# Kernel optimization log

Measured on AMD Instinct MI355X. Metric: run time of the kernel, lower is better.

The kernel has to match this reference:

```python
import jax, jax.numpy as jnp
import numpy as np


def setup_inputs() -> dict:
    key = jax.random.key(0)
    x = jax.random.normal(key, (8, 512, 96, 96), dtype=jnp.float32)
    gamma = jnp.zeros((1,), dtype=jnp.float32)  # Scale(0) learnable scalar
    return {"x": x, "gamma": gamma}


def reference(x, gamma):
    b, c, h, w = x.shape
    y = x.reshape(b, c, h * w)                      # [B, C, N]
    # channel-channel Gram matrix: [B, C, C]
    att = jnp.einsum('bcn,bdn->bcd', y, y)
    # DANet variant: softmax of (rowmax - scores)
    att = jnp.max(att, axis=-1, keepdims=True) - att
    att = jax.nn.softmax(att, axis=-1)
    # attention-weighted aggregation over channels: [B, C, N]
    feat = jnp.einsum('bcd,bdn->bcn', att, y).reshape(b, c, h, w)
    return gamma * feat + x
```

## Files before the change

kernel.cpp:

```cpp
#include <hip/hip_runtime.h>


typedef __attribute__((ext_vector_type(8))) short short8;
typedef __attribute__((ext_vector_type(4))) float f32x4;

#define GT 128
#define BK 64
#define LDA 72
#define NSPLIT 8
#define FBSPLIT 4

__device__ inline unsigned short f2bf(float f) {
    unsigned u = __builtin_bit_cast(unsigned, f);
    u += 0x7fffu + ((u >> 16) & 1u);
    return (unsigned short)(u >> 16);
}
__device__ inline unsigned permpack(float a, float b) {
    return __builtin_amdgcn_perm(__builtin_bit_cast(unsigned, b),
                                 __builtin_bit_cast(unsigned, a), 0x07060302u);
}
__device__ inline void gload_lds16(const short* g, short* l) {
    __builtin_amdgcn_global_load_lds(
        (const __attribute__((address_space(1))) void*)(g),
        (__attribute__((address_space(3))) void*)(l), 16, 0, 0);
}

__global__ __launch_bounds__(256) void tobf16_kernel(const float* __restrict__ x,
                                                     short* __restrict__ ybf) {
    const size_t total = (size_t)8 * 512 * 9216 / 8;
    const size_t stride = (size_t)gridDim.x * 256;
    for (size_t i = (size_t)blockIdx.x * 256 + threadIdx.x; i < total; i += stride) {
        const float4 a = ((const float4*)x)[2 * i];
        const float4 b = ((const float4*)x)[2 * i + 1];
        uint4 pv;
        pv.x = permpack(a.x, a.y);
        pv.y = permpack(a.z, a.w);
        pv.z = permpack(b.x, b.y);
        pv.w = permpack(b.z, b.w);
        ((uint4*)ybf)[i] = pv;
    }
}

__global__ __launch_bounds__(256, 2) void gram_kernel4(const short* __restrict__ ybf,
                                                       float* __restrict__ part) {
    const int C = 512, N = 9216;
    __shared__ short As[2][GT * BK];
    __shared__ short Bs[2][GT * BK];
    const int id = blockIdx.x;
    const int batch = id & 7;
    const int slot = id >> 3;
    const int split = slot / 10;
    const int pair = slot % 10;
    const int i_ = (pair < 4) ? 0 : (pair < 7) ? 1 : (pair < 9) ? 2 : 3;
    const int j_ = pair - ((i_ == 0) ? 0 : (i_ == 1) ? 3 : (i_ == 2) ? 5 : 6);
    const bool diag = (i_ == j_);
    const int c0 = i_ * GT, d0 = j_ * GT;
    const short* Y = ybf + (size_t)batch * C * N;
    const int t = threadIdx.x;
    const int w = t >> 6, l = t & 63;
    const int mw = (w >> 1) * 64, nw = (w & 1) * 64;
    const int lr = l & 15, lq = l >> 4;

    const int kw = N / NSPLIT;
    const int kbeg = split * kw;
    const int nt = kw / BK;

    auto STAGE = [&](int ti, int buf) {
        const int k0 = kbeg + ti * BK;
        #pragma unroll
        for (int p = 0; p < 4; ++p) {
            const int u = t + p * 256;
            const int row = u >> 3;
            const int us = (u ^ row) & 7;
            gload_lds16(Y + (size_t)(c0 + row) * N + k0 + us * 8, &As[buf][u * 8]);
        }
        if (!diag) {
            #pragma unroll
            for (int p = 0; p < 4; ++p) {
                const int u = t + p * 256;
                const int row = u >> 3;
                const int us = (u ^ row) & 7;
                gload_lds16(Y + (size_t)(d0 + row) * N + k0 + us * 8, &Bs[buf][u * 8]);
            }
        }
    };

    f32x4 acc[4][4] = {};
    STAGE(0, 0);
    __syncthreads();
    int cur = 0;
    for (int ti = 0; ti < nt; ++ti) {
        if (ti + 1 < nt) STAGE(ti + 1, cur ^ 1);
        const short* Acur = &As[cur][0];
        const short* Bcur = diag ? &As[cur][0] : &Bs[cur][0];
        #pragma unroll
        for (int h = 0; h < 2; ++h) {
            short8 af[4], bf[4];
            #pragma unroll
            for (int i = 0; i < 4; i++) {
                const int r = mw + i * 16 + lr;
                af[i] = *(const short8*)&Acur[r * BK + (((h * 4 + lq) ^ (r & 7)) * 8)];
            }
            #pragma unroll
            for (int j = 0; j < 4; j++) {
                const int r = nw + j * 16 + lr;
                bf[j] = *(const short8*)&Bcur[r * BK + (((h * 4 + lq) ^ (r & 7)) * 8)];
            }
            #pragma unroll
            for (int i = 0; i < 4; i++)
                #pragma unroll
                for (int j = 0; j < 4; j++)
                    acc[i][j] = __builtin_amdgcn_mfma_f32_16x16x32_bf16(af[i], bf[j], acc[i][j], 0, 0, 0);
        }
        __syncthreads();
        cur ^= 1;
    }
    float* P = part + ((size_t)batch * NSPLIT + split) * C * C;
    #pragma unroll
    for (int i = 0; i < 4; i++)
        #pragma unroll
        for (int j = 0; j < 4; j++)
            #pragma unroll
            for (int r = 0; r < 4; r++) {
                const int row = c0 + mw + i * 16 + lq * 4 + r;
                const int col = d0 + nw + j * 16 + lr;
                const float v = acc[i][j][r];
                P[(size_t)row * C + col] = v;
                if (!diag) P[(size_t)col * C + row] = v;
            }
}

__global__ __launch_bounds__(256) void rsoftmax_kernel(const float* __restrict__ part,
                                                       unsigned short* __restrict__ attbf) {
    const int C = 512;
    const int b = blockIdx.x >> 9;
    const int row = blockIdx.x & 511;
    const float* P0 = part + (size_t)b * NSPLIT * C * C + (size_t)row * C;
    const int t = threadIdx.x;
    float v0 = 0.f, v1 = 0.f;
    #pragma unroll
    for (int s = 0; s < NSPLIT; ++s) {
        const float* Ps = P0 + (size_t)s * C * C;
        v0 += Ps[t];
        v1 += Ps[t + 256];
    }

    float mn = fminf(v0, v1);
    #pragma unroll
    for (int off = 32; off > 0; off >>= 1) mn = fminf(mn, __shfl_xor(mn, off));
    __shared__ float redmin[4];
    const int wid = t >> 6, lane = t & 63;
    if (lane == 0) redmin[wid] = mn;
    __syncthreads();
    mn = fminf(fminf(redmin[0], redmin[1]), fminf(redmin[2], redmin[3]));

    const float e0 = expf(mn - v0), e1 = expf(mn - v1);
    float s = e0 + e1;
    #pragma unroll
    for (int off = 32; off > 0; off >>= 1) s += __shfl_xor(s, off);
    __shared__ float redsum[4];
    if (lane == 0) redsum[wid] = s;
    __syncthreads();
    s = redsum[0] + redsum[1] + redsum[2] + redsum[3];

    const float inv = 1.0f / s;
    unsigned short* A16 = attbf + (size_t)b * C * C + (size_t)row * C;
    A16[t] = f2bf(e0 * inv);
    A16[t + 256] = f2bf(e1 * inv);
}

__global__ __launch_bounds__(256, 2) void feat_kernel4(const short* __restrict__ attbf,
                                                       const short* __restrict__ ybf,
                                                       const float* __restrict__ x,
                                                       const float* __restrict__ gamma,
                                                       float* __restrict__ out) {
    const int C = 512, N = 9216;
    __shared__ short As[2][GT * BK];
    __shared__ short Bs[2][GT * BK];
    const int id = blockIdx.x;
    const int b = id & 7;
    const int slot = id >> 3;
    const int n0 = (slot >> 2) * GT;
    const int c0 = (slot & 3) * GT;
    const short* Ab = attbf + (size_t)b * C * C;
    const short* Y = ybf + (size_t)b * C * N;
    const int t = threadIdx.x;
    const int w = t >> 6, l = t & 63;
    const int mw = (w >> 1) * 64, nw = (w & 1) * 64;
    const int lr = l & 15, lq = l >> 4;
    const int ng = t & 31, kg = t >> 5;

    const int nt = C / BK;

    auto ASTAGE = [&](int ti, int buf) {
        const int k0 = ti * BK;
        #pragma unroll
        for (int p = 0; p < 4; ++p) {
            const int u = t + p * 256;
            const int row = u >> 3;
            const int us = (u ^ row) & 7;
            gload_lds16(Ab + (size_t)(c0 + row) * C + k0 + us * 8, &As[buf][u * 8]);
        }
    };

    uint2 rr[8];
    auto BLOAD = [&](int ti) {
        const short* pB = Y + (size_t)(ti * BK + kg * 8) * N + n0 + ng * 4;
        #pragma unroll
        for (int r = 0; r < 8; ++r) rr[r] = *(const uint2*)(pB + (size_t)r * N);
    };
    auto BWRITE = [&](int buf) {
        #pragma unroll
        for (int j = 0; j < 4; ++j) {
            const unsigned sel = (j & 1) ? 0x07060302u : 0x05040100u;
            unsigned w0, w1, w2, w3;
            if (j < 2) {
                w0 = __builtin_amdgcn_perm(rr[1].x, rr[0].x, sel);
                w1 = __builtin_amdgcn_perm(rr[3].x, rr[2].x, sel);
                w2 = __builtin_amdgcn_perm(rr[5].x, rr[4].x, sel);
                w3 = __builtin_amdgcn_perm(rr[7].x, rr[6].x, sel);
            } else {
                w0 = __builtin_amdgcn_perm(rr[1].y, rr[0].y, sel);
                w1 = __builtin_amdgcn_perm(rr[3].y, rr[2].y, sel);
                w2 = __builtin_amdgcn_perm(rr[5].y, rr[4].y, sel);
                w3 = __builtin_amdgcn_perm(rr[7].y, rr[6].y, sel);
            }
            const int nrow = ng * 4 + j;
            uint4 cv; cv.x = w0; cv.y = w1; cv.z = w2; cv.w = w3;
            *(uint4*)&Bs[buf][nrow * BK + ((kg ^ (nrow & 7)) * 8)] = cv;
        }
    };

    f32x4 acc[4][4] = {};
    BLOAD(0);
    ASTAGE(0, 0);
    BWRITE(0);
    __syncthreads();
    int cur = 0;
    for (int ti = 0; ti < nt; ++ti) {
        if (ti + 1 < nt) {
            BLOAD(ti + 1);
            ASTAGE(ti + 1, cur ^ 1);
        }
        #pragma unroll
        for (int h = 0; h < 2; ++h) {
            short8 af[4], bf[4];
            #pragma unroll
            for (int i = 0; i < 4; i++) {
                const int r = mw + i * 16 + lr;
                af[i] = *(const short8*)&As[cur][r * BK + (((h * 4 + lq) ^ (r & 7)) * 8)];
            }
            #pragma unroll
            for (int j = 0; j < 4; j++) {
                const int r = nw + j * 16 + lr;
                bf[j] = *(const short8*)&Bs[cur][r * BK + (((h * 4 + lq) ^ (r & 7)) * 8)];
            }
            #pragma unroll
            for (int i = 0; i < 4; i++)
                #pragma unroll
                for (int j = 0; j < 4; j++)
                    acc[i][j] = __builtin_amdgcn_mfma_f32_16x16x32_bf16(af[i], bf[j], acc[i][j], 0, 0, 0);
        }
        if (ti + 1 < nt) BWRITE(cur ^ 1);
        __syncthreads();
        cur ^= 1;
    }

    const float g = gamma[0];
    float* O = out + (size_t)b * C * N;
    const float* X = x + (size_t)b * C * N;
    #pragma unroll
    for (int i = 0; i < 4; i++)
        #pragma unroll
        for (int j = 0; j < 4; j++)
            #pragma unroll
            for (int r = 0; r < 4; r++) {
                const int row = c0 + mw + i * 16 + lq * 4 + r;
                const int col = n0 + nw + j * 16 + lr;
                const size_t idx = (size_t)row * N + col;
                O[idx] = g * acc[i][j][r] + X[idx];
            }
}

__global__ __launch_bounds__(256, 2) void gram_kernel3(const short* __restrict__ ybf,
                                                       float* __restrict__ att) {
    const int C = 512, N = 9216;
    __shared__ short As[2][GT * BK];
    __shared__ short Bs[2][GT * BK];
    const int id = blockIdx.x;
    const int batch = id & 7;
    const int slot = id >> 3;
    const int split = slot / 10;
    const int pair = slot % 10;
    const int i_ = (pair < 4) ? 0 : (pair < 7) ? 1 : (pair < 9) ? 2 : 3;
    const int j_ = pair - ((i_ == 0) ? 0 : (i_ == 1) ? 3 : (i_ == 2) ? 5 : 6);
    const bool diag = (i_ == j_);
    const int c0 = i_ * GT, d0 = j_ * GT;
    const short* Y = ybf + (size_t)batch * C * N;
    const int t = threadIdx.x;
    const int w = t >> 6, l = t & 63;
    const int mw = (w >> 1) * 64, nw = (w & 1) * 64;
    const int lr = l & 15, lq = l >> 4;

    const int kw = N / NSPLIT;
    const int kbeg = split * kw;
    const int nt = kw / BK;

    auto STAGE = [&](int ti, int buf) {
        const int k0 = kbeg + ti * BK;
        #pragma unroll
        for (int p = 0; p < 4; ++p) {
            const int u = t + p * 256;
            const int row = u >> 3;
            const int us = (u ^ row) & 7;
            gload_lds16(Y + (size_t)(c0 + row) * N + k0 + us * 8, &As[buf][u * 8]);
        }
        if (!diag) {
            #pragma unroll
            for (int p = 0; p < 4; ++p) {
                const int u = t + p * 256;
                const int row = u >> 3;
                const int us = (u ^ row) & 7;
                gload_lds16(Y + (size_t)(d0 + row) * N + k0 + us * 8, &Bs[buf][u * 8]);
            }
        }
    };

    f32x4 acc[4][4] = {};
    STAGE(0, 0);
    __syncthreads();
    int cur = 0;
    for (int ti = 0; ti < nt; ++ti) {
        if (ti + 1 < nt) STAGE(ti + 1, cur ^ 1);
        const short* Acur = &As[cur][0];
        const short* Bcur = diag ? &As[cur][0] : &Bs[cur][0];
        #pragma unroll
        for (int h = 0; h < 2; ++h) {
            short8 af[4], bf[4];
            #pragma unroll
            for (int i = 0; i < 4; i++) {
                const int r = mw + i * 16 + lr;
                af[i] = *(const short8*)&Acur[r * BK + (((h * 4 + lq) ^ (r & 7)) * 8)];
            }
            #pragma unroll
            for (int j = 0; j < 4; j++) {
                const int r = nw + j * 16 + lr;
                bf[j] = *(const short8*)&Bcur[r * BK + (((h * 4 + lq) ^ (r & 7)) * 8)];
            }
            #pragma unroll
            for (int i = 0; i < 4; i++)
                #pragma unroll
                for (int j = 0; j < 4; j++)
                    acc[i][j] = __builtin_amdgcn_mfma_f32_16x16x32_bf16(af[i], bf[j], acc[i][j], 0, 0, 0);
        }
        __syncthreads();
        cur ^= 1;
    }
    float* S = att + (size_t)batch * C * C;
    #pragma unroll
    for (int i = 0; i < 4; i++)
        #pragma unroll
        for (int j = 0; j < 4; j++)
            #pragma unroll
            for (int r = 0; r < 4; r++) {
                const int row = c0 + mw + i * 16 + lq * 4 + r;
                const int col = d0 + nw + j * 16 + lr;
                const float v = acc[i][j][r];
                unsafeAtomicAdd(&S[(size_t)row * C + col], v);
                if (!diag) unsafeAtomicAdd(&S[(size_t)col * C + row], v);
            }
}

__global__ __launch_bounds__(256) void softmax_kernel(float* __restrict__ att) {
    const int C = 512;
    float* S = att + (size_t)blockIdx.x * C;
    const int t = threadIdx.x;
    const float v0 = S[t], v1 = S[t + 256];

    float mn = fminf(v0, v1);
    #pragma unroll
    for (int off = 32; off > 0; off >>= 1) mn = fminf(mn, __shfl_xor(mn, off));
    __shared__ float redmin[4];
    const int wid = t >> 6, lane = t & 63;
    if (lane == 0) redmin[wid] = mn;
    __syncthreads();
    mn = fminf(fminf(redmin[0], redmin[1]), fminf(redmin[2], redmin[3]));

    const float e0 = expf(mn - v0), e1 = expf(mn - v1);
    float s = e0 + e1;
    #pragma unroll
    for (int off = 32; off > 0; off >>= 1) s += __shfl_xor(s, off);
    __shared__ float redsum[4];
    if (lane == 0) redsum[wid] = s;
    __syncthreads();
    s = redsum[0] + redsum[1] + redsum[2] + redsum[3];

    const float inv = 1.0f / s;
    unsigned short* S16 = (unsigned short*)S;
    S16[t] = f2bf(e0 * inv);
    S16[t + 256] = f2bf(e1 * inv);
}

__global__ __launch_bounds__(256, 2) void feat_kernel3(const float* __restrict__ att,
                                                       const short* __restrict__ ybf,
                                                       const float* __restrict__ x,
                                                       const float* __restrict__ gamma,
                                                       float* __restrict__ out) {
    const int C = 512, N = 9216;
    __shared__ short As[2][GT * BK];
    __shared__ short Bs[2][GT * BK];
    const int id = blockIdx.x;
    const int b = id & 7;
    const int slot = id >> 3;
    const int n0 = (slot >> 2) * GT;
    const int c0 = (slot & 3) * GT;
    const short* Ab = (const short*)(att + (size_t)b * C * C);
    const short* Y = ybf + (size_t)b * C * N;
    const int t = threadIdx.x;
    const int w = t >> 6, l = t & 63;
    const int mw = (w >> 1) * 64, nw = (w & 1) * 64;
    const int lr = l & 15, lq = l >> 4;
    const int ng = t & 31, kg = t >> 5;

    const int nt = C / BK;

    auto ASTAGE = [&](int ti, int buf) {
        const int k0 = ti * BK;
        #pragma unroll
        for (int p = 0; p < 4; ++p) {
            const int u = t + p * 256;
            const int row = u >> 3;
            const int us = (u ^ row) & 7;
            gload_lds16(Ab + (size_t)(c0 + row) * 1024 + k0 + us * 8, &As[buf][u * 8]);
        }
    };

    uint2 rr[8];
    auto BLOAD = [&](int ti) {
        const short* pB = Y + (size_t)(ti * BK + kg * 8) * N + n0 + ng * 4;
        #pragma unroll
        for (int r = 0; r < 8; ++r) rr[r] = *(const uint2*)(pB + (size_t)r * N);
    };
    auto BWRITE = [&](int buf) {
        #pragma unroll
        for (int j = 0; j < 4; ++j) {
            const unsigned sel = (j & 1) ? 0x07060302u : 0x05040100u;
            unsigned w0, w1, w2, w3;
            if (j < 2) {
                w0 = __builtin_amdgcn_perm(rr[1].x, rr[0].x, sel);
                w1 = __builtin_amdgcn_perm(rr[3].x, rr[2].x, sel);
                w2 = __builtin_amdgcn_perm(rr[5].x, rr[4].x, sel);
                w3 = __builtin_amdgcn_perm(rr[7].x, rr[6].x, sel);
            } else {
                w0 = __builtin_amdgcn_perm(rr[1].y, rr[0].y, sel);
                w1 = __builtin_amdgcn_perm(rr[3].y, rr[2].y, sel);
                w2 = __builtin_amdgcn_perm(rr[5].y, rr[4].y, sel);
                w3 = __builtin_amdgcn_perm(rr[7].y, rr[6].y, sel);
            }
            const int nrow = ng * 4 + j;
            uint4 cv; cv.x = w0; cv.y = w1; cv.z = w2; cv.w = w3;
            *(uint4*)&Bs[buf][nrow * BK + ((kg ^ (nrow & 7)) * 8)] = cv;
        }
    };

    f32x4 acc[4][4] = {};
    BLOAD(0);
    ASTAGE(0, 0);
    BWRITE(0);
    __syncthreads();
    int cur = 0;
    for (int ti = 0; ti < nt; ++ti) {
        if (ti + 1 < nt) {
            BLOAD(ti + 1);
            ASTAGE(ti + 1, cur ^ 1);
        }
        #pragma unroll
        for (int h = 0; h < 2; ++h) {
            short8 af[4], bf[4];
            #pragma unroll
            for (int i = 0; i < 4; i++) {
                const int r = mw + i * 16 + lr;
                af[i] = *(const short8*)&As[cur][r * BK + (((h * 4 + lq) ^ (r & 7)) * 8)];
            }
            #pragma unroll
            for (int j = 0; j < 4; j++) {
                const int r = nw + j * 16 + lr;
                bf[j] = *(const short8*)&Bs[cur][r * BK + (((h * 4 + lq) ^ (r & 7)) * 8)];
            }
            #pragma unroll
            for (int i = 0; i < 4; i++)
                #pragma unroll
                for (int j = 0; j < 4; j++)
                    acc[i][j] = __builtin_amdgcn_mfma_f32_16x16x32_bf16(af[i], bf[j], acc[i][j], 0, 0, 0);
        }
        if (ti + 1 < nt) BWRITE(cur ^ 1);
        __syncthreads();
        cur ^= 1;
    }

    const float g = gamma[0];
    float* O = out + (size_t)b * C * N;
    const float* X = x + (size_t)b * C * N;
    #pragma unroll
    for (int i = 0; i < 4; i++)
        #pragma unroll
        for (int j = 0; j < 4; j++)
            #pragma unroll
            for (int r = 0; r < 4; r++) {
                const int row = c0 + mw + i * 16 + lq * 4 + r;
                const int col = n0 + nw + j * 16 + lr;
                const size_t idx = (size_t)row * N + col;
                O[idx] = g * acc[i][j][r] + X[idx];
            }
}

__global__ __launch_bounds__(256, 2) void gram_fb(const float* __restrict__ x,
                                                  float* __restrict__ att,
                                                  int C, int N) {
    __shared__ short As[GT * LDA];
    __shared__ short Bs[GT * LDA];
    const int bz = blockIdx.z;
    const int batch = bz & 7, split = bz >> 3;
    const int c0 = blockIdx.y * GT;
    const int d0 = blockIdx.x * GT;
    const float* Y = x + (size_t)batch * C * N;
    const int t = threadIdx.x;
    const int w = t >> 6, l = t & 63;
    const int mw = (w >> 1) * 64, nw = (w & 1) * 64;
    const int lr = l & 15, lq = l >> 4;

    f32x4 acc[4][4] = {};
    const int kbeg = split * (N / FBSPLIT);
    const int kend = kbeg + (N / FBSPLIT);
    for (int k0 = kbeg; k0 < kend; k0 += BK) {
        #pragma unroll
        for (int i = 0; i < 8; i++) {
            const int v = t + i * 256;
            const int row = v >> 4, kq = v & 15;
            float4 a = *(const float4*)(Y + (size_t)(c0 + row) * N + k0 + kq * 4);
            uint2 pa = make_uint2(permpack(a.x, a.y), permpack(a.z, a.w));
            *(uint2*)&As[row * LDA + kq * 4] = pa;
            float4 bv = *(const float4*)(Y + (size_t)(d0 + row) * N + k0 + kq * 4);
            uint2 pb = make_uint2(permpack(bv.x, bv.y), permpack(bv.z, bv.w));
            *(uint2*)&Bs[row * LDA + kq * 4] = pb;
        }
        __syncthreads();
        #pragma unroll
        for (int h = 0; h < 2; h++) {
            short8 af[4], bf[4];
            #pragma unroll
            for (int i = 0; i < 4; i++)
                af[i] = *(short8*)&As[(mw + i * 16 + lr) * LDA + h * 32 + lq * 8];
            #pragma unroll
            for (int j = 0; j < 4; j++)
                bf[j] = *(short8*)&Bs[(nw + j * 16 + lr) * LDA + h * 32 + lq * 8];
            #pragma unroll
            for (int i = 0; i < 4; i++)
                #pragma unroll
                for (int j = 0; j < 4; j++)
                    acc[i][j] = __builtin_amdgcn_mfma_f32_16x16x32_bf16(af[i], bf[j], acc[i][j], 0, 0, 0);
        }
        __syncthreads();
    }
    float* S = att + (size_t)batch * C * C;
    #pragma unroll
    for (int i = 0; i < 4; i++)
        #pragma unroll
        for (int j = 0; j < 4; j++)
            #pragma unroll
            for (int r = 0; r < 4; r++) {
                const int row = c0 + mw + i * 16 + lq * 4 + r;
                const int col = d0 + nw + j * 16 + lr;
                unsafeAtomicAdd(&S[(size_t)row * C + col], acc[i][j][r]);
            }
}

__global__ __launch_bounds__(256, 2) void feat_fb(const float* __restrict__ att,
                                                  const float* __restrict__ x,
                                                  const float* __restrict__ gamma,
                                                  float* __restrict__ out,
                                                  int C, int N) {
    __shared__ short As[GT * LDA];
    __shared__ short Bs[GT * LDA];
    const int b  = blockIdx.z;
    const int c0 = blockIdx.y * GT;
    const int n0 = blockIdx.x * GT;
    const short* Ab = (const short*)(att + (size_t)b * C * C);
    const float* Y = x + (size_t)b * C * N;
    const int t = threadIdx.x;
    const int w = t >> 6, l = t & 63;
    const int mw = (w >> 1) * 64, nw = (w & 1) * 64;
    const int lr = l & 15, lq = l >> 4;

    f32x4 acc[4][4] = {};
    for (int k0 = 0; k0 < C; k0 += BK) {
        #pragma unroll
        for (int i = 0; i < 4; i++) {
            const int v = t + i * 256;
            const int row = v >> 3, q = v & 7;
            uint4 va = *(const uint4*)(Ab + (size_t)(c0 + row) * 1024 + k0 + q * 8);
            *(uint4*)&As[row * LDA + q * 8] = va;
        }
        #pragma unroll
        for (int i = 0; i < 2; i++) {
            const int v = t + i * 256;
            const int kg = v & 15, ng = v >> 4;
            const float* p0 = Y + (size_t)(k0 + kg * 4) * N + n0 + ng * 4;
            float4 r0 = *(const float4*)(p0);
            float4 r1 = *(const float4*)(p0 + N);
            float4 r2 = *(const float4*)(p0 + 2 * (size_t)N);
            float4 r3 = *(const float4*)(p0 + 3 * (size_t)N);
            const float j0[4] = {r0.x, r1.x, r2.x, r3.x};
            const float j1[4] = {r0.y, r1.y, r2.y, r3.y};
            const float j2[4] = {r0.z, r1.z, r2.z, r3.z};
            const float j3[4] = {r0.w, r1.w, r2.w, r3.w};
            const float* cols[4] = {j0, j1, j2, j3};
            #pragma unroll
            for (int j = 0; j < 4; j++) {
                uint2 p = make_uint2(permpack(cols[j][0], cols[j][1]),
                                     permpack(cols[j][2], cols[j][3]));
                *(uint2*)&Bs[(ng * 4 + j) * LDA + kg * 4] = p;
            }
        }
        __syncthreads();
        #pragma unroll
        for (int h = 0; h < 2; h++) {
            short8 af[4], bf[4];
            #pragma unroll
            for (int i = 0; i < 4; i++)
                af[i] = *(short8*)&As[(mw + i * 16 + lr) * LDA + h * 32 + lq * 8];
            #pragma unroll
            for (int j = 0; j < 4; j++)
                bf[j] = *(short8*)&Bs[(nw + j * 16 + lr) * LDA + h * 32 + lq * 8];
            #pragma unroll
            for (int i = 0; i < 4; i++)
                #pragma unroll
                for (int j = 0; j < 4; j++)
                    acc[i][j] = __builtin_amdgcn_mfma_f32_16x16x32_bf16(af[i], bf[j], acc[i][j], 0, 0, 0);
        }
        __syncthreads();
    }

    const float g = gamma[0];
    float* O = out + (size_t)b * C * N;
    const float* X = x + (size_t)b * C * N;
    #pragma unroll
    for (int i = 0; i < 4; i++)
        #pragma unroll
        for (int j = 0; j < 4; j++)
            #pragma unroll
            for (int r = 0; r < 4; r++) {
                const int row = c0 + mw + i * 16 + lq * 4 + r;
                const int col = n0 + nw + j * 16 + lr;
                const size_t idx = (size_t)row * N + col;
                O[idx] = g * acc[i][j][r] + X[idx];
            }
}

extern "C" void kernel_launch(void* const* d_in, const int* in_sizes, int n_in,
                              void* d_out, int out_size, void* d_ws, size_t ws_size,
                              hipStream_t stream) {
    const int B = 8, C = 512, N = 96 * 96;
    const float* x     = (const float*)d_in[0];
    const float* gamma = (const float*)d_in[1];
    float* out = (float*)d_out;
    const size_t attBytes  = (size_t)B * C * C * sizeof(float);
    const size_t ybfBytes  = (size_t)B * C * N * sizeof(short);
    const size_t partBytes = (size_t)B * NSPLIT * C * C * sizeof(float);

    dim3 blk(256);
    if (ws_size >= attBytes + ybfBytes + partBytes) {
        unsigned short* attbf = (unsigned short*)d_ws;
        short* ybf  = (short*)((char*)d_ws + attBytes);
        float* part = (float*)((char*)d_ws + attBytes + ybfBytes);
        tobf16_kernel<<<2048, blk, 0, stream>>>(x, ybf);
        gram_kernel4<<<dim3(8 * NSPLIT * 10), blk, 0, stream>>>(ybf, part);
        rsoftmax_kernel<<<dim3(B * C), blk, 0, stream>>>(part, attbf);
        feat_kernel4<<<dim3(8 * 288), blk, 0, stream>>>((const short*)attbf, ybf, x, gamma, out);
    } else if (ws_size >= attBytes + ybfBytes) {
        float* att = (float*)d_ws;
        short* ybf = (short*)((char*)d_ws + attBytes);
        hipMemsetAsync(att, 0, attBytes, stream);
        tobf16_kernel<<<2048, blk, 0, stream>>>(x, ybf);
        gram_kernel3<<<dim3(8 * NSPLIT * 10), blk, 0, stream>>>(ybf, att);
        softmax_kernel<<<dim3(B * C), blk, 0, stream>>>(att);
        feat_kernel3<<<dim3(8 * 288), blk, 0, stream>>>(att, ybf, x, gamma, out);
    } else {
        float* att = (float*)d_ws;
        hipMemsetAsync(att, 0, attBytes, stream);
        gram_fb<<<dim3(C / GT, C / GT, B * FBSPLIT), blk, 0, stream>>>(x, att, C, N);
        softmax_kernel<<<dim3(B * C), blk, 0, stream>>>(att);
        feat_fb<<<dim3(N / GT, C / GT, B), blk, 0, stream>>>(att, x, gamma, out, C, N);
    }
}
```

Baseline: 426.6 us.

## Precompute transposed bf16 activations so feature GEMM streams both operands directly

```diff
diff --git a/kernel.cpp b/kernel.cpp
--- a/kernel.cpp
+++ b/kernel.cpp
@@ -18,6 +18,12 @@
 __device__ inline unsigned permpack(float a, float b) {
     return __builtin_amdgcn_perm(__builtin_bit_cast(unsigned, b),
                                  __builtin_bit_cast(unsigned, a), 0x07060302u);
+}
+__device__ inline unsigned permlo(unsigned lo, unsigned hi) {
+    return __builtin_amdgcn_perm(hi, lo, 0x05040100u);
+}
+__device__ inline unsigned permhi(unsigned lo, unsigned hi) {
+    return __builtin_amdgcn_perm(hi, lo, 0x07060302u);
 }
 __device__ inline void gload_lds16(const short* g, short* l) {
     __builtin_amdgcn_global_load_lds(
@@ -39,6 +45,57 @@
         pv.w = permpack(b.z, b.w);
         ((uint4*)ybf)[i] = pv;
     }
+}
+
+__global__ __launch_bounds__(256) void convtr_kernel(const float* __restrict__ x,
+                                                     short* __restrict__ ybf,
+                                                     short* __restrict__ ytr) {
+    const int C = 512, N = 9216;
+    const int b = blockIdx.z, cB = blockIdx.y * 64, nB = blockIdx.x * 64;
+    const int t = threadIdx.x, ca = t & 15, nb = t >> 4;
+    const float* X = x + ((size_t)b * C + cB) * N + nB;
+    float4 v[4];
+    #pragma unroll
+    for (int r = 0; r < 4; ++r)
+        v[r] = *(const float4*)(X + (size_t)(ca * 4 + r) * N + nb * 4);
+    short* Yb = ybf + ((size_t)b * C + cB) * N + nB;
+    #pragma unroll
+    for (int r = 0; r < 4; ++r) {
+        uint2 p = make_uint2(permpack(v[r].x, v[r].y), permpack(v[r].z, v[r].w));
+        *(uint2*)(Yb + (size_t)(ca * 4 + r) * N + nb * 4) = p;
+    }
+    short* Yt = ytr + ((size_t)b * N + nB) * C + cB;
+    {
+        uint2 p0 = make_uint2(permpack(v[0].x, v[1].x), permpack(v[2].x, v[3].x));
+        uint2 p1 = make_uint2(permpack(v[0].y, v[1].y), permpack(v[2].y, v[3].y));
+        uint2 p2 = make_uint2(permpack(v[0].z, v[1].z), permpack(v[2].z, v[3].z));
+        uint2 p3 = make_uint2(permpack(v[0].w, v[1].w), permpack(v[2].w, v[3].w));
+        *(uint2*)(Yt + (size_t)(nb * 4 + 0) * C + ca * 4) = p0;
+        *(uint2*)(Yt + (size_t)(nb * 4 + 1) * C + ca * 4) = p1;
+        *(uint2*)(Yt + (size_t)(nb * 4 + 2) * C + ca * 4) = p2;
+        *(uint2*)(Yt + (size_t)(nb * 4 + 3) * C + ca * 4) = p3;
+    }
+}
+
+__global__ __launch_bounds__(256) void trbf_kernel(const short* __restrict__ ybf,
+                                                   short* __restrict__ ytr) {
+    const int C = 512, N = 9216;
+    const int b = blockIdx.z, cB = blockIdx.y * 64, nB = blockIdx.x * 64;
+    const int t = threadIdx.x, ca = t & 15, nb = t >> 4;
+    const short* Yb = ybf + ((size_t)b * C + cB) * N + nB;
+    uint2 rr[4];
+    #pragma unroll
+    for (int r = 0; r < 4; ++r)
+        rr[r] = *(const uint2*)(Yb + (size_t)(ca * 4 + r) * N + nb * 4);
+    short* Yt = ytr + ((size_t)b * N + nB) * C + cB;
+    uint2 p0 = make_uint2(permlo(rr[0].x, rr[1].x), permlo(rr[2].x, rr[3].x));
+    uint2 p1 = make_uint2(permhi(rr[0].x, rr[1].x), permhi(rr[2].x, rr[3].x));
+    uint2 p2 = make_uint2(permlo(rr[0].y, rr[1].y), permlo(rr[2].y, rr[3].y));
+    uint2 p3 = make_uint2(permhi(rr[0].y, rr[1].y), permhi(rr[2].y, rr[3].y));
+    *(uint2*)(Yt + (size_t)(nb * 4 + 0) * C + ca * 4) = p0;
+    *(uint2*)(Yt + (size_t)(nb * 4 + 1) * C + ca * 4) = p1;
+    *(uint2*)(Yt + (size_t)(nb * 4 + 2) * C + ca * 4) = p2;
+    *(uint2*)(Yt + (size_t)(nb * 4 + 3) * C + ca * 4) = p3;
 }
 
 __global__ __launch_bounds__(256, 2) void gram_kernel4(const short* __restrict__ ybf,
@@ -167,6 +224,91 @@
     unsigned short* A16 = attbf + (size_t)b * C * C + (size_t)row * C;
     A16[t] = f2bf(e0 * inv);
     A16[t + 256] = f2bf(e1 * inv);
+}
+
+__global__ __launch_bounds__(256, 2) void feat_kernel5(const short* __restrict__ attbf,
+                                                       const short* __restrict__ ytr,
+                                                       const float* __restrict__ x,
+                                                       const float* __restrict__ gamma,
+                                                       float* __restrict__ out) {
+    const int C = 512, N = 9216;
+    __shared__ short As[2][GT * BK];
+    __shared__ short Bs[2][GT * BK];
+    const int id = blockIdx.x;
+    const int b = id & 7;
+    const int slot = id >> 3;
+    const int n0 = (slot >> 2) * GT;
+    const int c0 = (slot & 3) * GT;
+    const short* Ab = attbf + (size_t)b * C * C;
+    const short* Yt = ytr + (size_t)b * N * C;
+    const int t = threadIdx.x;
+    const int w = t >> 6, l = t & 63;
+    const int mw = (w >> 1) * 64, nw = (w & 1) * 64;
+    const int lr = l & 15, lq = l >> 4;
+
+    const int nt = C / BK;
+
+    auto STAGE = [&](int ti, int buf) {
+        const int k0 = ti * BK;
+        #pragma unroll
+        for (int p = 0; p < 4; ++p) {
+            const int u = t + p * 256;
+            const int row = u >> 3;
+            const int us = (u ^ row) & 7;
+            gload_lds16(Ab + (size_t)(c0 + row) * C + k0 + us * 8, &As[buf][u * 8]);
+        }
+        #pragma unroll
+        for (int p = 0; p < 4; ++p) {
+            const int u = t + p * 256;
+            const int row = u >> 3;
+            const int us = (u ^ row) & 7;
+            gload_lds16(Yt + (size_t)(n0 + row) * C + k0 + us * 8, &Bs[buf][u * 8]);
+        }
+    };
+
+    f32x4 acc[4][4] = {};
+    STAGE(0, 0);
+    __syncthreads();
+    int cur = 0;
+    for (int ti = 0; ti < nt; ++ti) {
+        if (ti + 1 < nt) STAGE(ti + 1, cur ^ 1);
+        #pragma unroll
+        for (int h = 0; h < 2; ++h) {
+            short8 af[4], bf[4];
+            #pragma unroll
+            for (int i = 0; i < 4; i++) {
+                const int r = mw + i * 16 + lr;
+                af[i] = *(const short8*)&As[cur][r * BK + (((h * 4 + lq) ^ (r & 7)) * 8)];
+            }
+            #pragma unroll
+            for (int j = 0; j < 4; j++) {
+                const int r = nw + j * 16 + lr;
+                bf[j] = *(const short8*)&Bs[cur][r * BK + (((h * 4 + lq) ^ (r & 7)) * 8)];
+            }
+            #pragma unroll
+            for (int i = 0; i < 4; i++)
+                #pragma unroll
+                for (int j = 0; j < 4; j++)
+                    acc[i][j] = __builtin_amdgcn_mfma_f32_16x16x32_bf16(af[i], bf[j], acc[i][j], 0, 0, 0);
+        }
+        __syncthreads();
+        cur ^= 1;
+    }
+
+    const float g = gamma[0];
+    float* O = out + (size_t)b * C * N;
+    const float* X = x + (size_t)b * C * N;
+    #pragma unroll
+    for (int i = 0; i < 4; i++)
+        #pragma unroll
+        for (int j = 0; j < 4; j++)
+            #pragma unroll
+            for (int r = 0; r < 4; r++) {
+                const int row = c0 + mw + i * 16 + lq * 4 + r;
+                const int col = n0 + nw + j * 16 + lr;
+                const size_t idx = (size_t)row * N + col;
+                O[idx] = g * acc[i][j][r] + X[idx];
+            }
 }
 
 __global__ __launch_bounds__(256, 2) void feat_kernel4(const short* __restrict__ attbf,
@@ -282,238 +424,6 @@
             }
 }
 
-__global__ __launch_bounds__(256, 2) void gram_kernel3(const short* __restrict__ ybf,
-                                                       float* __restrict__ att) {
-    const int C = 512, N = 9216;
-    __shared__ short As[2][GT * BK];
-    __shared__ short Bs[2][GT * BK];
-    const int id = blockIdx.x;
-    const int batch = id & 7;
-    const int slot = id >> 3;
-    const int split = slot / 10;
-    const int pair = slot % 10;
-    const int i_ = (pair < 4) ? 0 : (pair < 7) ? 1 : (pair < 9) ? 2 : 3;
-    const int j_ = pair - ((i_ == 0) ? 0 : (i_ == 1) ? 3 : (i_ == 2) ? 5 : 6);
-    const bool diag = (i_ == j_);
-    const int c0 = i_ * GT, d0 = j_ * GT;
-    const short* Y = ybf + (size_t)batch * C * N;
-    const int t = threadIdx.x;
-    const int w = t >> 6, l = t & 63;
-    const int mw = (w >> 1) * 64, nw = (w & 1) * 64;
-    const int lr = l & 15, lq = l >> 4;
-
-    const int kw = N / NSPLIT;
-    const int kbeg = split * kw;
-    const int nt = kw / BK;
-
-    auto STAGE = [&](int ti, int buf) {
-        const int k0 = kbeg + ti * BK;
-        #pragma unroll
-        for (int p = 0; p < 4; ++p) {
-            const int u = t + p * 256;
-            const int row = u >> 3;
-            const int us = (u ^ row) & 7;
-            gload_lds16(Y + (size_t)(c0 + row) * N + k0 + us * 8, &As[buf][u * 8]);
-        }
-        if (!diag) {
-            #pragma unroll
-            for (int p = 0; p < 4; ++p) {
-                const int u = t + p * 256;
-                const int row = u >> 3;
-                const int us = (u ^ row) & 7;
-                gload_lds16(Y + (size_t)(d0 + row) * N + k0 + us * 8, &Bs[buf][u * 8]);
-            }
-        }
-    };
-
-    f32x4 acc[4][4] = {};
-    STAGE(0, 0);
-    __syncthreads();
-    int cur = 0;
-    for (int ti = 0; ti < nt; ++ti) {
-        if (ti + 1 < nt) STAGE(ti + 1, cur ^ 1);
-        const short* Acur = &As[cur][0];
-        const short* Bcur = diag ? &As[cur][0] : &Bs[cur][0];
-        #pragma unroll
-        for (int h = 0; h < 2; ++h) {
-            short8 af[4], bf[4];
-            #pragma unroll
-            for (int i = 0; i < 4; i++) {
-                const int r = mw + i * 16 + lr;
-                af[i] = *(const short8*)&Acur[r * BK + (((h * 4 + lq) ^ (r & 7)) * 8)];
-            }
-            #pragma unroll
-            for (int j = 0; j < 4; j++) {
-                const int r = nw + j * 16 + lr;
-                bf[j] = *(const short8*)&Bcur[r * BK + (((h * 4 + lq) ^ (r & 7)) * 8)];
-            }
-            #pragma unroll
-            for (int i = 0; i < 4; i++)
-                #pragma unroll
-                for (int j = 0; j < 4; j++)
-                    acc[i][j] = __builtin_amdgcn_mfma_f32_16x16x32_bf16(af[i], bf[j], acc[i][j], 0, 0, 0);
-        }
-        __syncthreads();
-        cur ^= 1;
-    }
-    float* S = att + (size_t)batch * C * C;
-    #pragma unroll
-    for (int i = 0; i < 4; i++)
-        #pragma unroll
-        for (int j = 0; j < 4; j++)
-            #pragma unroll
-            for (int r = 0; r < 4; r++) {
-                const int row = c0 + mw + i * 16 + lq * 4 + r;
-                const int col = d0 + nw + j * 16 + lr;
-                const float v = acc[i][j][r];
-                unsafeAtomicAdd(&S[(size_t)row * C + col], v);
-                if (!diag) unsafeAtomicAdd(&S[(size_t)col * C + row], v);
-            }
-}
-
-__global__ __launch_bounds__(256) void softmax_kernel(float* __restrict__ att) {
-    const int C = 512;
-    float* S = att + (size_t)blockIdx.x * C;
-    const int t = threadIdx.x;
-    const float v0 = S[t], v1 = S[t + 256];
-
-    float mn = fminf(v0, v1);
-    #pragma unroll
-    for (int off = 32; off > 0; off >>= 1) mn = fminf(mn, __shfl_xor(mn, off));
-    __shared__ float redmin[4];
-    const int wid = t >> 6, lane = t & 63;
-    if (lane == 0) redmin[wid] = mn;
-    __syncthreads();
-    mn = fminf(fminf(redmin[0], redmin[1]), fminf(redmin[2], redmin[3]));
-
-    const float e0 = expf(mn - v0), e1 = expf(mn - v1);
-    float s = e0 + e1;
-    #pragma unroll
-    for (int off = 32; off > 0; off >>= 1) s += __shfl_xor(s, off);
-    __shared__ float redsum[4];
-    if (lane == 0) redsum[wid] = s;
-    __syncthreads();
-    s = redsum[0] + redsum[1] + redsum[2] + redsum[3];
-
-    const float inv = 1.0f / s;
-    unsigned short* S16 = (unsigned short*)S;
-    S16[t] = f2bf(e0 * inv);
-    S16[t + 256] = f2bf(e1 * inv);
-}
-
-__global__ __launch_bounds__(256, 2) void feat_kernel3(const float* __restrict__ att,
-                                                       const short* __restrict__ ybf,
-                                                       const float* __restrict__ x,
-                                                       const float* __restrict__ gamma,
-                                                       float* __restrict__ out) {
-    const int C = 512, N = 9216;
-    __shared__ short As[2][GT * BK];
-    __shared__ short Bs[2][GT * BK];
-    const int id = blockIdx.x;
-    const int b = id & 7;
-    const int slot = id >> 3;
-    const int n0 = (slot >> 2) * GT;
-    const int c0 = (slot & 3) * GT;
-    const short* Ab = (const short*)(att + (size_t)b * C * C);
-    const short* Y = ybf + (size_t)b * C * N;
-    const int t = threadIdx.x;
-    const int w = t >> 6, l = t & 63;
-    const int mw = (w >> 1) * 64, nw = (w & 1) * 64;
-    const int lr = l & 15, lq = l >> 4;
-    const int ng = t & 31, kg = t >> 5;
-
-    const int nt = C / BK;
-
-    auto ASTAGE = [&](int ti, int buf) {
-        const int k0 = ti * BK;
-        #pragma unroll
-        for (int p = 0; p < 4; ++p) {
-            const int u = t + p * 256;
-            const int row = u >> 3;
-            const int us = (u ^ row) & 7;
-            gload_lds16(Ab + (size_t)(c0 + row) * 1024 + k0 + us * 8, &As[buf][u * 8]);
-        }
-    };
-
-    uint2 rr[8];
-    auto BLOAD = [&](int ti) {
-        const short* pB = Y + (size_t)(ti * BK + kg * 8) * N + n0 + ng * 4;
-        #pragma unroll
-        for (int r = 0; r < 8; ++r) rr[r] = *(const uint2*)(pB + (size_t)r * N);
-    };
-    auto BWRITE = [&](int buf) {
-        #pragma unroll
-        for (int j = 0; j < 4; ++j) {
-            const unsigned sel = (j & 1) ? 0x07060302u : 0x05040100u;
-            unsigned w0, w1, w2, w3;
-            if (j < 2) {
-                w0 = __builtin_amdgcn_perm(rr[1].x, rr[0].x, sel);
-                w1 = __builtin_amdgcn_perm(rr[3].x, rr[2].x, sel);
-                w2 = __builtin_amdgcn_perm(rr[5].x, rr[4].x, sel);
-                w3 = __builtin_amdgcn_perm(rr[7].x, rr[6].x, sel);
-            } else {
-                w0 = __builtin_amdgcn_perm(rr[1].y, rr[0].y, sel);
-                w1 = __builtin_amdgcn_perm(rr[3].y, rr[2].y, sel);
-                w2 = __builtin_amdgcn_perm(rr[5].y, rr[4].y, sel);
-                w3 = __builtin_amdgcn_perm(rr[7].y, rr[6].y, sel);
-            }
-            const int nrow = ng * 4 + j;
-            uint4 cv; cv.x = w0; cv.y = w1; cv.z = w2; cv.w = w3;
-            *(uint4*)&Bs[buf][nrow * BK + ((kg ^ (nrow & 7)) * 8)] = cv;
-        }
-    };
-
-    f32x4 acc[4][4] = {};
-    BLOAD(0);
-    ASTAGE(0, 0);
-    BWRITE(0);
-    __syncthreads();
-    int cur = 0;
-    for (int ti = 0; ti < nt; ++ti) {
-        if (ti + 1 < nt) {
-            BLOAD(ti + 1);
-            ASTAGE(ti + 1, cur ^ 1);
-        }
-        #pragma unroll
-        for (int h = 0; h < 2; ++h) {
-            short8 af[4], bf[4];
-            #pragma unroll
-            for (int i = 0; i < 4; i++) {
-                const int r = mw + i * 16 + lr;
-                af[i] = *(const short8*)&As[cur][r * BK + (((h * 4 + lq) ^ (r & 7)) * 8)];
-            }
-            #pragma unroll
-            for (int j = 0; j < 4; j++) {
-                const int r = nw + j * 16 + lr;
-                bf[j] = *(const short8*)&Bs[cur][r * BK + (((h * 4 + lq) ^ (r & 7)) * 8)];
-            }
-            #pragma unroll
-            for (int i = 0; i < 4; i++)
-                #pragma unroll
-                for (int j = 0; j < 4; j++)
-                    acc[i][j] = __builtin_amdgcn_mfma_f32_16x16x32_bf16(af[i], bf[j], acc[i][j], 0, 0, 0);
-        }
-        if (ti + 1 < nt) BWRITE(cur ^ 1);
-        __syncthreads();
-        cur ^= 1;
-    }
-
-    const float g = gamma[0];
-    float* O = out + (size_t)b * C * N;
-    const float* X = x + (size_t)b * C * N;
-    #pragma unroll
-    for (int i = 0; i < 4; i++)
-        #pragma unroll
-        for (int j = 0; j < 4; j++)
-            #pragma unroll
-            for (int r = 0; r < 4; r++) {
-                const int row = c0 + mw + i * 16 + lq * 4 + r;
-                const int col = n0 + nw + j * 16 + lr;
-                const size_t idx = (size_t)row * N + col;
-                O[idx] = g * acc[i][j][r] + X[idx];
-            }
-}
-
 __global__ __launch_bounds__(256, 2) void gram_fb(const float* __restrict__ x,
                                                   float* __restrict__ att,
                                                   int C, int N) {
@@ -573,6 +483,36 @@
                 const int col = d0 + nw + j * 16 + lr;
                 unsafeAtomicAdd(&S[(size_t)row * C + col], acc[i][j][r]);
             }
+}
+
+__global__ __launch_bounds__(256) void softmax_kernel(float* __restrict__ att) {
+    const int C = 512;
+    float* S = att + (size_t)blockIdx.x * C;
+    const int t = threadIdx.x;
+    const float v0 = S[t], v1 = S[t + 256];
+
+    float mn = fminf(v0, v1);
+    #pragma unroll
+    for (int off = 32; off > 0; off >>= 1) mn = fminf(mn, __shfl_xor(mn, off));
+    __shared__ float redmin[4];
+    const int wid = t >> 6, lane = t & 63;
+    if (lane == 0) redmin[wid] = mn;
+    __syncthreads();
+    mn = fminf(fminf(redmin[0], redmin[1]), fminf(redmin[2], redmin[3]));
+
+    const float e0 = expf(mn - v0), e1 = expf(mn - v1);
+    float s = e0 + e1;
+    #pragma unroll
+    for (int off = 32; off > 0; off >>= 1) s += __shfl_xor(s, off);
+    __shared__ float redsum[4];
+    if (lane == 0) redsum[wid] = s;
+    __syncthreads();
+    s = redsum[0] + redsum[1] + redsum[2] + redsum[3];
+
+    const float inv = 1.0f / s;
+    unsigned short* S16 = (unsigned short*)S;
+    S16[t] = f2bf(e0 * inv);
+    S16[t + 256] = f2bf(e1 * inv);
 }
 
 __global__ __launch_bounds__(256, 2) void feat_fb(const float* __restrict__ att,
@@ -666,10 +606,31 @@
     float* out = (float*)d_out;
     const size_t attBytes  = (size_t)B * C * C * sizeof(float);
     const size_t ybfBytes  = (size_t)B * C * N * sizeof(short);
+    const size_t ytrBytes  = (size_t)B * N * C * sizeof(short);
     const size_t partBytes = (size_t)B * NSPLIT * C * C * sizeof(float);
 
     dim3 blk(256);
-    if (ws_size >= attBytes + ybfBytes + partBytes) {
+    if (ws_size >= attBytes + ybfBytes + ytrBytes + partBytes) {
+        unsigned short* attbf = (unsigned short*)d_ws;
+        short* ybf  = (short*)((char*)d_ws + attBytes);
+        short* ytr  = (short*)((char*)d_ws + attBytes + ybfBytes);
+        float* part = (float*)((char*)d_ws + attBytes + ybfBytes + ytrBytes);
+        convtr_kernel<<<dim3(N / 64, C / 64, B), blk, 0, stream>>>(x, ybf, ytr);
+        gram_kernel4<<<dim3(8 * NSPLIT * 10), blk, 0, stream>>>(ybf, part);
+        rsoftmax_kernel<<<dim3(B * C), blk, 0, stream>>>(part, attbf);
+        feat_kernel5<<<dim3(8 * 288), blk, 0, stream>>>((const short*)attbf, ytr, x, gamma, out);
+    } else if (ws_size >= attBytes + ybfBytes + ytrBytes) {
+        unsigned short* attbf = (unsigned short*)d_ws;
+        short* ybf  = (short*)((char*)d_ws + attBytes);
+        char* region = (char*)d_ws + attBytes + ybfBytes;
+        float* part = (float*)region;
+        short* ytr  = (short*)region;
+        tobf16_kernel<<<2048, blk, 0, stream>>>(x, ybf);
+        gram_kernel4<<<dim3(8 * NSPLIT * 10), blk, 0, stream>>>(ybf, part);
+        rsoftmax_kernel<<<dim3(B * C), blk, 0, stream>>>(part, attbf);
+        trbf_kernel<<<dim3(N / 64, C / 64, B), blk, 0, stream>>>(ybf, ytr);
+        feat_kernel5<<<dim3(8 * 288), blk, 0, stream>>>((const short*)attbf, ytr, x, gamma, out);
+    } else if (ws_size >= attBytes + ybfBytes + partBytes) {
         unsigned short* attbf = (unsigned short*)d_ws;
         short* ybf  = (short*)((char*)d_ws + attBytes);
         float* part = (float*)((char*)d_ws + attBytes + ybfBytes);
@@ -677,14 +638,6 @@
         gram_kernel4<<<dim3(8 * NSPLIT * 10), blk, 0, stream>>>(ybf, part);
         rsoftmax_kernel<<<dim3(B * C), blk, 0, stream>>>(part, attbf);
         feat_kernel4<<<dim3(8 * 288), blk, 0, stream>>>((const short*)attbf, ybf, x, gamma, out);
-    } else if (ws_size >= attBytes + ybfBytes) {
-        float* att = (float*)d_ws;
-        short* ybf = (short*)((char*)d_ws + attBytes);
-        hipMemsetAsync(att, 0, attBytes, stream);
-        tobf16_kernel<<<2048, blk, 0, stream>>>(x, ybf);
-        gram_kernel3<<<dim3(8 * NSPLIT * 10), blk, 0, stream>>>(ybf, att);
-        softmax_kernel<<<dim3(B * C), blk, 0, stream>>>(att);
-        feat_kernel3<<<dim3(8 * 288), blk, 0, stream>>>(att, ybf, x, gamma, out);
     } else {
         float* att = (float*)d_ws;
         hipMemsetAsync(att, 0, attBytes, stream);
```

New measurement: 452.7 us. 6.1% more time.
